# Performance work log

Measured on AMD Instinct MI355X. Metric: run time of the kernel, lower is better.

Reference implementation:

```python
import jax, jax.numpy as jnp
import numpy as np

N, E, R, D = 50000, 640000, 200, 128  # nodes, edges, relations, feat dim (in_feat==out_feat)
EPS = 1e-5  # LayerNorm eps
NEG_SLOPE = 0.01  # F.leaky_relu default

def _xavier(k, shape):
    gain = np.sqrt(2.0)  # calculate_gain('relu')
    std = gain * np.sqrt(2.0 / (shape[0] + shape[1]))
    a = np.sqrt(3.0) * std
    return jax.random.uniform(k, shape, jnp.float32, -a, a)

def setup_inputs() -> dict:
    key = jax.random.key(0)
    ks = jax.random.split(key, 10)
    return {
        "node": jax.random.normal(ks[0], (N, D), jnp.float32),
        "rel": jax.random.normal(ks[1], (R, D), jnp.float32),
        "norm": jax.random.uniform(ks[2], (N, 1), jnp.float32),
        "w_triplet": _xavier(ks[3], (3 * D, D)),
        "w_quad": _xavier(ks[4], (D, D)),
        "loop_weight": _xavier(ks[5], (D, D)),
        "evolve_loop_weight": _xavier(ks[6], (D, D)),
        "src": jax.random.randint(ks[7], (E,), 0, N),
        "dst": jax.random.randint(ks[8], (E,), 0, N),
        "etype": jax.random.randint(ks[9], (E,), 0, R),
    }

def reference(node, rel, norm, w_triplet, w_quad, loop_weight, evolve_loop_weight, src, dst, etype):
    # triplet = cat([h_src, rel_emb, h_dst], 1) @ w_triplet, computed blockwise
    # to avoid materializing the [E, 3D] concat.
    W_s, W_r, W_d = w_triplet[:D], w_triplet[D:2 * D], w_triplet[2 * D:]
    triplet = node[src] @ W_s + rel[etype] @ W_r + node[dst] @ W_d  # [E, D]
    # 'fre' not in edata -> sro_fre is zeros; a_triplet = triplet @ w_quad
    a = jax.nn.leaky_relu(triplet @ w_quad, negative_slope=NEG_SLOPE)  # [E, D]
    # edge_softmax: softmax over incoming edges per destination node, per feature
    a_max = jax.ops.segment_max(a, dst, num_segments=N)
    a_max = jnp.where(jnp.isfinite(a_max), a_max, 0.0)  # empty segments -> -inf
    ex = jnp.exp(a - a_max[dst])
    denom = jax.ops.segment_sum(ex, dst, num_segments=N)
    att = ex / denom[dst]
    # weighted scatter-sum aggregation, then apply_func: h * norm
    h = jax.ops.segment_sum(att * triplet, dst, num_segments=N) * norm  # [N, D]
    # self-loop: evolve_loop_weight for in-degree-0 nodes, loop_weight otherwise
    indeg = jax.ops.segment_sum(jnp.ones((E,), jnp.float32), dst, num_segments=N)
    loop = jnp.where((indeg > 0)[:, None], node @ loop_weight, node @ evolve_loop_weight)
    out = h + loop
    # LayerNorm(elementwise_affine=False)
    mu = jnp.mean(out, axis=-1, keepdims=True)
    var = jnp.var(out, axis=-1, keepdims=True)
    return (out - mu) * jax.lax.rsqrt(var + EPS)
```

## Files before the change

kernel.cpp:

```cpp
#include <hip/hip_runtime.h>
#include <hip/hip_bf16.h>

#define D 128
#define LOG2E 1.4426950408889634f

typedef __attribute__((ext_vector_type(8))) short bf16x8;
typedef __attribute__((ext_vector_type(4))) float f32x4;
typedef __attribute__((ext_vector_type(2))) float f32x2;
typedef __attribute__((ext_vector_type(2))) unsigned u32x2;
typedef __attribute__((ext_vector_type(4))) unsigned u32x4;

__device__ __forceinline__ unsigned short f2bf_bits(float f) {
    union { __hip_bfloat16 h; unsigned short u; } c;
    c.h = __float2bfloat16(f);
    return c.u;
}
__device__ __forceinline__ float bfbits2f(unsigned short u) {
    return __uint_as_float(((unsigned)u) << 16);
}
__device__ __forceinline__ float ldf(const void* p, size_t i, int f32) {
    return f32 ? ((const float*)p)[i] : bfbits2f(((const unsigned short*)p)[i]);
}
__device__ __forceinline__ f32x2 unpk2(unsigned u) {
    f32x2 r;
    r.x = __uint_as_float(u << 16);
    r.y = __uint_as_float(u & 0xFFFF0000u);
    return r;
}
__device__ __forceinline__ f32x2 shx32(f32x2 v) {
    f32x2 r;
    r.x = __shfl_xor(v.x, 32);
    r.y = __shfl_xor(v.y, 32);
    return r;
}
__device__ __forceinline__ f32x2 pk_add(f32x2 a, f32x2 b) {
    f32x2 d;
    asm("v_pk_add_f32 %0, %1, %2" : "=v"(d) : "v"(a), "v"(b));
    return d;
}
__device__ __forceinline__ f32x2 pk_mul(f32x2 a, f32x2 b) {
    f32x2 d;
    asm("v_pk_mul_f32 %0, %1, %2" : "=v"(d) : "v"(a), "v"(b));
    return d;
}
__device__ __forceinline__ f32x2 pk_fma(f32x2 a, f32x2 b, f32x2 c) {
    f32x2 d;
    asm("v_pk_fma_f32 %0, %1, %2, %3" : "=v"(d) : "v"(a), "v"(b), "v"(c));
    return d;
}
__device__ __forceinline__ float fexp2(float x) {
    float r;
    asm("v_exp_f32 %0, %1" : "=v"(r) : "v"(x));
    return r;
}

__global__ __launch_bounds__(256) void prep_kernel(
    const void* __restrict__ node, const void* __restrict__ wtrip,
    const void* __restrict__ wquad, const void* __restrict__ loopW,
    const void* __restrict__ evoW, unsigned short* __restrict__ wT,
    int* __restrict__ cnt, int* __restrict__ rank,
    const int* __restrict__ dst, int* __restrict__ flag, int E) {
    __shared__ int sflag;
    int tid = threadIdx.x;
    int bad = 0;
    if (tid < 64) {
        for (int j = 0; j < 4; j++) {
            float v = bfbits2f(((const unsigned short*)node)[tid + 64 * j]);
            if (!(fabsf(v) < 1e4f)) bad = 1;
        }
    }
    unsigned long long m = __ballot(bad);
    if (tid == 0) sflag = (m != 0ull) ? 1 : 0;
    __syncthreads();
    int f32 = sflag;
    int bx = blockIdx.x;
    if (bx == 0 && tid == 0) *flag = f32;

    if (bx < 192) {
        int unit = bx * 2 + (tid >> 7);
        int k = unit & 127, mjob = unit >> 7;
        int t = tid & 127;
        float acc = 0.f;
        for (int j = 0; j < D; j++)
            acc += ldf(wtrip, (size_t)mjob * D * D + (size_t)k * D + j, f32) *
                   ldf(wquad, (size_t)j * D + t, f32);
        const int jmap0 = (mjob == 0) ? 0 : (mjob == 1 ? 6 : 2);
        wT[(size_t)jmap0 * D * D + (size_t)t * D + k] = f2bf_bits(acc);
    } else if (bx < 272) {
        int u = bx - 192;
        int jr = u >> 4, seg = u & 15;
        const void* srcp; size_t base; int j;
        switch (jr) {
            case 0: srcp = wtrip; base = 0;             j = 1; break;
            case 1: srcp = wtrip; base = 2 * D * D;     j = 3; break;
            case 2: srcp = loopW; base = 0;             j = 4; break;
            case 3: srcp = evoW;  base = 0;             j = 5; break;
            default: srcp = wtrip; base = (size_t)D * D; j = 7; break;
        }
        for (int c = tid; c < 1024; c += 256) {
            int idx = seg * 1024 + c;
            int n = idx >> 7, k = idx & 127;
            unsigned short b = f32 ? f2bf_bits(((const float*)srcp)[base + (size_t)k * D + n])
                                   : ((const unsigned short*)srcp)[base + (size_t)k * D + n];
            wT[(size_t)j * D * D + (size_t)n * D + k] = b;
        }
    } else {
        int e = (bx - 272) * 256 + tid;
        if (e < E) rank[e] = atomicAdd(&cnt[dst[e]], 1);
    }
}

__global__ void scan_block(const int* __restrict__ cnt, int* __restrict__ offs,
                           int* __restrict__ part, int N) {
    __shared__ int sh[256];
    int tid = threadIdx.x;
    int i = blockIdx.x * 256 + tid;
    int v = (i < N) ? cnt[i] : 0;
    sh[tid] = v;
    __syncthreads();
    for (int o = 1; o < 256; o <<= 1) {
        int t = (tid >= o) ? sh[tid - o] : 0;
        __syncthreads();
        sh[tid] += t;
        __syncthreads();
    }
    if (i < N) offs[i] = sh[tid] - v;
    if (tid == 255) part[blockIdx.x] = sh[255];
}

__global__ void scan_fix(int* __restrict__ offs, const int* __restrict__ part,
                         int N, int E) {
    __shared__ int sh[256];
    int tid = threadIdx.x, b = blockIdx.x;
    sh[tid] = (tid < b) ? part[tid] : 0;
    __syncthreads();
    for (int o = 128; o; o >>= 1) {
        if (tid < o) sh[tid] += sh[tid + o];
        __syncthreads();
    }
    int carry = sh[0];
    int i = b * 256 + tid;
    if (i < N) offs[i] += carry;
    if (b == 0 && tid == 0) offs[N] = E;
}

__global__ __launch_bounds__(512) void gemm_kernel(
    const void* __restrict__ node, const void* __restrict__ rel,
    const unsigned short* __restrict__ wT, const int* __restrict__ cnt,
    unsigned* __restrict__ nodeST, unsigned* __restrict__ nodeDT,
    unsigned* __restrict__ relRT, unsigned* __restrict__ loopSel,
    const int* __restrict__ flag, int N, int R, int nodeBlocks,
    const int* __restrict__ src, const int* __restrict__ dst,
    const int* __restrict__ et, const int* __restrict__ offs,
    const int* __restrict__ rank, unsigned* __restrict__ ePack, int E) {
    __shared__ __align__(16) unsigned short Wt[D][D + 8];

    int bx = blockIdx.x, by = blockIdx.y;
    int tid = threadIdx.y * 64 + threadIdx.x;
    int isRel = 0, jp;
    if (bx >= nodeBlocks) {
        if (by == 1) {
            int e = (bx - nodeBlocks) * 512 + tid;
            if (e < E) {
                int d = dst[e];
                ePack[offs[d] + rank[e]] = (unsigned)src[e] | ((unsigned)et[e] << 20);
            }
            return;
        }
        if (by != 0 || bx - nodeBlocks >= (R + 127) / 128) return;
        isRel = 1;
        jp = 3;
    } else {
        jp = by;
    }

    int f32 = *flag;
    int rows = isRel ? R : N;
    int row0 = (isRel ? bx - nodeBlocks : bx) * 128;
    const void* A = isRel ? rel : node;

    int lane = threadIdx.x, wv = threadIdx.y;
    int l16 = lane & 15, quad = lane >> 4;
    int ar = row0 + wv * 16 + l16;
    int ar_c = ar < rows ? ar : rows - 1;

    int qIdx, tIdx;
    unsigned* O = nullptr;
    switch (jp) {
        case 0: qIdx = 0; tIdx = 1; O = nodeST; break;
        case 1: qIdx = 2; tIdx = 3; O = nodeDT; break;
        case 2: qIdx = 4; tIdx = 5; break;
        default: qIdx = 6; tIdx = 7; O = relRT; break;
    }

    bf16x8 af[4];
#pragma unroll
    for (int kk = 0; kk < 4; kk++) {
        int k = kk * 32 + quad * 8;
        if (f32) {
            const float* Af = (const float*)A + (size_t)ar_c * D + k;
            float4 x0 = *(const float4*)(Af);
            float4 x1 = *(const float4*)(Af + 4);
            af[kk][0] = (short)f2bf_bits(x0.x);
            af[kk][1] = (short)f2bf_bits(x0.y);
            af[kk][2] = (short)f2bf_bits(x0.z);
            af[kk][3] = (short)f2bf_bits(x0.w);
            af[kk][4] = (short)f2bf_bits(x1.x);
            af[kk][5] = (short)f2bf_bits(x1.y);
            af[kk][6] = (short)f2bf_bits(x1.z);
            af[kk][7] = (short)f2bf_bits(x1.w);
        } else {
            af[kk] = *(const bf16x8*)((const unsigned short*)A + (size_t)ar_c * D + k);
        }
    }

    const unsigned short* gQ = wT + (size_t)qIdx * D * D;
    const unsigned short* gT = wT + (size_t)tIdx * D * D;

    bf16x8 wreg[4], wreg2[4];
#pragma unroll
    for (int i = 0; i < 4; i++) {
        int c = tid + i * 512;
        wreg[i] = *(const bf16x8*)(gQ + (c >> 4) * 128 + (c & 15) * 8);
    }

    f32x4 accQ[8], accT[8];
#pragma unroll
    for (int i = 0; i < 8; i++) {
        accQ[i] = (f32x4){0.f, 0.f, 0.f, 0.f};
        accT[i] = (f32x4){0.f, 0.f, 0.f, 0.f};
    }

    for (int pass = 0; pass < 2; pass++) {
#pragma unroll
        for (int i = 0; i < 4; i++) {
            int c = tid + i * 512;
            *(bf16x8*)(&Wt[c >> 4][(c & 15) * 8]) = wreg[i];
        }
        if (pass == 0) {
#pragma unroll
            for (int i = 0; i < 4; i++) {
                int c = tid + i * 512;
                wreg2[i] = *(const bf16x8*)(gT + (c >> 4) * 128 + (c & 15) * 8);
            }
        }
        __syncthreads();
        f32x4* acc = pass ? accT : accQ;
#pragma unroll
        for (int kk = 0; kk < 4; kk++) {
#pragma unroll
            for (int nt = 0; nt < 8; nt++) {
                bf16x8 bfr = *(const bf16x8*)(&Wt[nt * 16 + l16][kk * 32 + quad * 8]);
                acc[nt] = __builtin_amdgcn_mfma_f32_16x16x32_bf16(af[kk], bfr, acc[nt], 0, 0, 0);
            }
        }
        __syncthreads();
#pragma unroll
        for (int i = 0; i < 4; i++) wreg[i] = wreg2[i];
    }

    int cr0 = row0 + wv * 16 + quad * 4;
    int odd = l16 & 1;
    if (jp != 2) {
#pragma unroll
        for (int r = 0; r < 4; r++) {
            int cr = cr0 + r;
#pragma unroll
            for (int nt = 0; nt < 8; nt++) {
                float vQ = accQ[nt][r] * LOG2E;
                float vT = accT[nt][r];
                float oQ = __shfl_xor(vQ, 1);
                float oT = __shfl_xor(vT, 1);
                unsigned w;
                if (!odd) w = (unsigned)f2bf_bits(vQ) | ((unsigned)f2bf_bits(oQ) << 16);
                else      w = (unsigned)f2bf_bits(oT) | ((unsigned)f2bf_bits(vT) << 16);
                if (cr < rows) O[(size_t)cr * 128 + nt * 16 + l16] = w;
            }
        }
    } else {
#pragma unroll
        for (int r = 0; r < 4; r++) {
            int cr = cr0 + r;
            int deg = (cr < rows) ? cnt[cr] : 0;
#pragma unroll
            for (int nt = 0; nt < 8; nt++) {
                float vL = accQ[nt][r], vE = accT[nt][r];
                float oL = __shfl_xor(vL, 1);
                float oE = __shfl_xor(vE, 1);
                unsigned wl, we;
                if (!odd) {
                    wl = (unsigned)f2bf_bits(vL) | ((unsigned)f2bf_bits(oL) << 16);
                    we = (unsigned)f2bf_bits(vE) | ((unsigned)f2bf_bits(oE) << 16);
                } else {
                    wl = (unsigned)f2bf_bits(oL) | ((unsigned)f2bf_bits(vL) << 16);
                    we = (unsigned)f2bf_bits(oE) | ((unsigned)f2bf_bits(vE) << 16);
                }
                if (cr < rows && !odd)
                    loopSel[(size_t)cr * 64 + nt * 8 + (l16 >> 1)] = (deg > 0) ? wl : we;
            }
        }
    }
}

__global__ __launch_bounds__(256) void agg_kernel(
    const int* __restrict__ offs, const unsigned* __restrict__ ePack,
    const unsigned* __restrict__ ST, const unsigned* __restrict__ RT,
    const unsigned* __restrict__ DT, const unsigned* __restrict__ loopSel,
    const void* __restrict__ normv, void* __restrict__ out,
    const int* __restrict__ flag, int N) {
    int n = blockIdx.x * 4 + threadIdx.y;
    if (n >= N) return;
    int f32 = *flag;
    int lane = threadIdx.x;
    int half = lane >> 5, sl = lane & 31;
    int start = offs[n], end = offs[n + 1];
    int deg = end - start;

    u32x4 ud = *(const u32x4*)(DT + (size_t)n * 128 + sl * 4);
    f32x2 qd01 = unpk2(ud.x), td01 = unpk2(ud.y);
    f32x2 qd23 = unpk2(ud.z), td23 = unpk2(ud.w);
    u32x2 ul = *(const u32x2*)(loopSel + (size_t)n * 64 + sl * 2);
    f32x2 acc01 = unpk2(ul.x), acc23 = unpk2(ul.y);

    const char* STb = (const char*)ST;
    const char* RTb = (const char*)RT;
    unsigned laneoff = (unsigned)(sl * 16);

    f32x2 den01 = {0.f, 0.f}, den23 = {0.f, 0.f};
    f32x2 h01 = {0.f, 0.f}, h23 = {0.f, 0.f};
    const f32x2 ns2 = {0.01f, 0.01f};

#define GLOAD(PK, US, UR)                                                   \
    u32x4 US = *(const u32x4*)(STb + ((((PK) & 0xFFFFFu) << 9) + laneoff)); \
    u32x4 UR = *(const u32x4*)(RTb + ((((PK) >> 20) << 9) + laneoff));

#define EMATH(US, UR)                                                       \
    {                                                                       \
        f32x2 q01 = pk_add(pk_add(unpk2(US.x), unpk2(UR.x)), qd01);         \
        f32x2 q23 = pk_add(pk_add(unpk2(US.z), unpk2(UR.z)), qd23);         \
        f32x2 s01 = pk_mul(q01, ns2);                                       \
        f32x2 s23 = pk_mul(q23, ns2);                                       \
        f32x2 ex01, ex23;                                                   \
        ex01.x = fexp2(fmaxf(q01.x, s01.x));                                \
        ex01.y = fexp2(fmaxf(q01.y, s01.y));                                \
        ex23.x = fexp2(fmaxf(q23.x, s23.x));                                \
        ex23.y = fexp2(fmaxf(q23.y, s23.y));                                \
        den01 = pk_add(den01, ex01); den23 = pk_add(den23, ex23);           \
        f32x2 t01 = pk_add(pk_add(unpk2(US.y), unpk2(UR.y)), td01);         \
        f32x2 t23 = pk_add(pk_add(unpk2(US.w), unpk2(UR.w)), td23);         \
        h01 = pk_fma(ex01, t01, h01);                                       \
        h23 = pk_fma(ex23, t23, h23);                                       \
    }

#define EMATHV(US, UR, VM)                                                  \
    {                                                                       \
        f32x2 q01 = pk_add(pk_add(unpk2(US.x), unpk2(UR.x)), qd01);         \
        f32x2 q23 = pk_add(pk_add(unpk2(US.z), unpk2(UR.z)), qd23);         \
        f32x2 s01 = pk_mul(q01, ns2);                                       \
        f32x2 s23 = pk_mul(q23, ns2);                                       \
        f32x2 ex01, ex23;                                                   \
        ex01.x = fexp2(fmaxf(q01.x, s01.x)) * (VM);                         \
        ex01.y = fexp2(fmaxf(q01.y, s01.y)) * (VM);                         \
        ex23.x = fexp2(fmaxf(q23.x, s23.x)) * (VM);                         \
        ex23.y = fexp2(fmaxf(q23.y, s23.y)) * (VM);                         \
        den01 = pk_add(den01, ex01); den23 = pk_add(den23, ex23);           \
        f32x2 t01 = pk_add(pk_add(unpk2(US.y), unpk2(UR.y)), td01);         \
        f32x2 t23 = pk_add(pk_add(unpk2(US.w), unpk2(UR.w)), td23);         \
        h01 = pk_fma(ex01, t01, h01);                                       \
        h23 = pk_fma(ex23, t23, h23);                                       \
    }

    int e = start;
    for (; e + 3 < end; e += 4) {
        unsigned pA = ePack[e + half];
        unsigned pB = ePack[e + 2 + half];
        GLOAD(pA, usA, urA)
        GLOAD(pB, usB, urB)
        EMATH(usA, urA)
        EMATH(usB, urB)
    }
    for (; e < end; e += 2) {
        int eh = e + half;
        int valid = eh < end;
        unsigned pT = ePack[valid ? eh : end - 1];
        GLOAD(pT, usT, urT)
        EMATHV(usT, urT, valid ? 1.0f : 0.0f)
    }
#undef GLOAD
#undef EMATH
#undef EMATHV

    den01 = pk_add(den01, shx32(den01)); den23 = pk_add(den23, shx32(den23));
    h01 = pk_add(h01, shx32(h01));       h23 = pk_add(h23, shx32(h23));

    f32x2 x01, x23;
    if (deg > 0) {
        float nrm = ldf(normv, n, f32);
        x01 = h01 / den01 * nrm + acc01;
        x23 = h23 / den23 * nrm + acc23;
    } else {
        x01 = acc01;
        x23 = acc23;
    }

    float s = (x01.x + x01.y) + (x23.x + x23.y);
    float ss = (x01.x * x01.x + x01.y * x01.y) + (x23.x * x23.x + x23.y * x23.y);
#pragma unroll
    for (int o = 16; o; o >>= 1) {
        s += __shfl_xor(s, o);
        ss += __shfl_xor(ss, o);
    }
    float mu = s * (1.f / 128.f);
    float var = ss * (1.f / 128.f) - mu * mu;
    float rstd = rsqrtf(var + 1e-5f);
    f32x2 y01 = (x01 - mu) * rstd;
    f32x2 y23 = (x23 - mu) * rstd;

    if (half == 0) {
        if (f32) {
            float4 o4 = make_float4(y01.x, y01.y, y23.x, y23.y);
            ((float4*)out)[(size_t)n * 32 + sl] = o4;
        } else {
            u32x2 ow;
            ow.x = (unsigned)f2bf_bits(y01.x) | ((unsigned)f2bf_bits(y01.y) << 16);
            ow.y = (unsigned)f2bf_bits(y23.x) | ((unsigned)f2bf_bits(y23.y) << 16);
            *(u32x2*)((unsigned*)out + (size_t)n * 64 + sl * 2) = ow;
        }
    }
}

extern "C" void kernel_launch(void* const* d_in, const int* in_sizes, int n_in,
                              void* d_out, int out_size, void* d_ws, size_t ws_size,
                              hipStream_t stream) {
    const void* node = d_in[0];
    const void* rel = d_in[1];
    const void* normv = d_in[2];
    const void* wtrip = d_in[3];
    const void* wquad = d_in[4];
    const void* loopW = d_in[5];
    const void* evoW = d_in[6];
    const int* src = (const int*)d_in[7];
    const int* dst = (const int*)d_in[8];
    const int* et = (const int*)d_in[9];

    int N = in_sizes[0] / D;
    int R = in_sizes[1] / D;
    int E = in_sizes[7];
    int nb = (N + 255) / 256;
    int nodeBlocks = (N + 127) / 128;
    int relBlocks = (R + 127) / 128;
    int scatBlocks = (E + 511) / 512;

    char* p = (char*)d_ws;
    auto alloc = [&](size_t bytes) -> void* {
        void* r = (void*)p;
        p += (bytes + 255) & ~(size_t)255;
        return r;
    };
    unsigned* nodeST = (unsigned*)alloc((size_t)N * 128 * 4);
    unsigned* nodeDT = (unsigned*)alloc((size_t)N * 128 * 4);
    unsigned* relRT = (unsigned*)alloc((size_t)R * 128 * 4);
    unsigned* loopSel = (unsigned*)alloc((size_t)N * 64 * 4);
    unsigned short* wT = (unsigned short*)alloc((size_t)8 * D * D * 2);
    int* cnt = (int*)alloc((size_t)N * 4);
    int* offs = (int*)alloc((size_t)(N + 1) * 4);
    int* part = (int*)alloc((size_t)(nb + 1) * 4);
    int* rank = (int*)alloc((size_t)E * 4);
    unsigned* ePack = (unsigned*)alloc((size_t)E * 4);
    int* flag = (int*)alloc(4);

    hipMemsetAsync(cnt, 0, (size_t)N * 4, stream);
    prep_kernel<<<272 + (E + 255) / 256, 256, 0, stream>>>(
        node, wtrip, wquad, loopW, evoW, wT, cnt, rank, dst, flag, E);
    scan_block<<<nb, 256, 0, stream>>>(cnt, offs, part, N);
    scan_fix<<<nb, 256, 0, stream>>>(offs, part, N, E);
    int xext = nodeBlocks + (scatBlocks > relBlocks ? scatBlocks : relBlocks);
    gemm_kernel<<<dim3(xext, 3), dim3(64, 8), 0, stream>>>(
        node, rel, wT, cnt, nodeST, nodeDT, relRT, loopSel, flag, N, R, nodeBlocks,
        src, dst, et, offs, rank, ePack, E);
    agg_kernel<<<(N + 3) / 4, dim3(64, 4), 0, stream>>>(
        offs, ePack, nodeST, relRT, nodeDT, loopSel, normv, d_out, flag, N);
}
```

Baseline: 233.6 us.

## Compute all three node projections per block and pre-shift packed edge indices

The gemm kernel now uses a 1D grid. Each node block loads its A-row fragment once and loops over six weight matrices in sequence, writing the ST, DT and loop outputs one after another, instead of launching three separate y-blocks that each reload and convert the node rows. The edge pack grows from 32 to 64 bits and stores the src and etype offsets already shifted, so agg_kernel skips the mask and shift arithmetic per edge. The cost is three times fewer node blocks, each doing three times the work, which lowers parallelism, and twice the bytes for ePack reads and writes.

```diff
diff --git a/kernel.cpp b/kernel.cpp
--- a/kernel.cpp
+++ b/kernel.cpp
@@ -149,30 +149,26 @@
     const unsigned short* __restrict__ wT, const int* __restrict__ cnt,
     unsigned* __restrict__ nodeST, unsigned* __restrict__ nodeDT,
     unsigned* __restrict__ relRT, unsigned* __restrict__ loopSel,
-    const int* __restrict__ flag, int N, int R, int nodeBlocks,
+    const int* __restrict__ flag, int N, int R, int nodeBlocks, int relBlocks,
     const int* __restrict__ src, const int* __restrict__ dst,
     const int* __restrict__ et, const int* __restrict__ offs,
-    const int* __restrict__ rank, unsigned* __restrict__ ePack, int E) {
+    const int* __restrict__ rank, u32x2* __restrict__ ePack, int E) {
     __shared__ __align__(16) unsigned short Wt[D][D + 8];
 
-    int bx = blockIdx.x, by = blockIdx.y;
+    int bx = blockIdx.x;
     int tid = threadIdx.y * 64 + threadIdx.x;
-    int isRel = 0, jp;
-    if (bx >= nodeBlocks) {
-        if (by == 1) {
-            int e = (bx - nodeBlocks) * 512 + tid;
-            if (e < E) {
-                int d = dst[e];
-                ePack[offs[d] + rank[e]] = (unsigned)src[e] | ((unsigned)et[e] << 20);
-            }
-            return;
-        }
-        if (by != 0 || bx - nodeBlocks >= (R + 127) / 128) return;
-        isRel = 1;
-        jp = 3;
-    } else {
-        jp = by;
-    }
+    if (bx >= nodeBlocks + relBlocks) {
+        int e = (bx - nodeBlocks - relBlocks) * 512 + tid;
+        if (e < E) {
+            int d = dst[e];
+            u32x2 pk;
+            pk.x = ((unsigned)src[e]) << 9;
+            pk.y = ((unsigned)et[e]) << 9;
+            ePack[offs[d] + rank[e]] = pk;
+        }
+        return;
+    }
+    int isRel = bx >= nodeBlocks;
 
     int f32 = *flag;
     int rows = isRel ? R : N;
@@ -183,15 +179,6 @@
     int l16 = lane & 15, quad = lane >> 4;
     int ar = row0 + wv * 16 + l16;
     int ar_c = ar < rows ? ar : rows - 1;
-
-    int qIdx, tIdx;
-    unsigned* O = nullptr;
-    switch (jp) {
-        case 0: qIdx = 0; tIdx = 1; O = nodeST; break;
-        case 1: qIdx = 2; tIdx = 3; O = nodeDT; break;
-        case 2: qIdx = 4; tIdx = 5; break;
-        default: qIdx = 6; tIdx = 7; O = relRT; break;
-    }
 
     bf16x8 af[4];
 #pragma unroll
@@ -214,14 +201,14 @@
         }
     }
 
-    const unsigned short* gQ = wT + (size_t)qIdx * D * D;
-    const unsigned short* gT = wT + (size_t)tIdx * D * D;
+    const int base = isRel ? 6 : 0;
+    const int npass = isRel ? 2 : 6;
 
     bf16x8 wreg[4], wreg2[4];
 #pragma unroll
     for (int i = 0; i < 4; i++) {
         int c = tid + i * 512;
-        wreg[i] = *(const bf16x8*)(gQ + (c >> 4) * 128 + (c & 15) * 8);
+        wreg[i] = *(const bf16x8*)(wT + (size_t)base * D * D + (c >> 4) * 128 + (c & 15) * 8);
     }
 
     f32x4 accQ[8], accT[8];
@@ -231,21 +218,25 @@
         accT[i] = (f32x4){0.f, 0.f, 0.f, 0.f};
     }
 
-    for (int pass = 0; pass < 2; pass++) {
+    int cr0 = row0 + wv * 16 + quad * 4;
+    int odd = l16 & 1;
+
+    for (int s = 0; s < npass; s++) {
 #pragma unroll
         for (int i = 0; i < 4; i++) {
             int c = tid + i * 512;
             *(bf16x8*)(&Wt[c >> 4][(c & 15) * 8]) = wreg[i];
         }
-        if (pass == 0) {
+        if (s + 1 < npass) {
+            const unsigned short* gN = wT + (size_t)(base + s + 1) * D * D;
 #pragma unroll
             for (int i = 0; i < 4; i++) {
                 int c = tid + i * 512;
-                wreg2[i] = *(const bf16x8*)(gT + (c >> 4) * 128 + (c & 15) * 8);
+                wreg2[i] = *(const bf16x8*)(gN + (c >> 4) * 128 + (c & 15) * 8);
             }
         }
         __syncthreads();
-        f32x4* acc = pass ? accT : accQ;
+        f32x4* acc = (s & 1) ? accT : accQ;
 #pragma unroll
         for (int kk = 0; kk < 4; kk++) {
 #pragma unroll
@@ -257,53 +248,62 @@
         __syncthreads();
 #pragma unroll
         for (int i = 0; i < 4; i++) wreg[i] = wreg2[i];
-    }
-
-    int cr0 = row0 + wv * 16 + quad * 4;
-    int odd = l16 & 1;
-    if (jp != 2) {
-#pragma unroll
-        for (int r = 0; r < 4; r++) {
-            int cr = cr0 + r;
-#pragma unroll
-            for (int nt = 0; nt < 8; nt++) {
-                float vQ = accQ[nt][r] * LOG2E;
-                float vT = accT[nt][r];
-                float oQ = __shfl_xor(vQ, 1);
-                float oT = __shfl_xor(vT, 1);
-                unsigned w;
-                if (!odd) w = (unsigned)f2bf_bits(vQ) | ((unsigned)f2bf_bits(oQ) << 16);
-                else      w = (unsigned)f2bf_bits(oT) | ((unsigned)f2bf_bits(vT) << 16);
-                if (cr < rows) O[(size_t)cr * 128 + nt * 16 + l16] = w;
+
+        if (s & 1) {
+            int job = s >> 1;
+            if (isRel || job < 2) {
+                unsigned* O = isRel ? relRT : (job == 0 ? nodeST : nodeDT);
+#pragma unroll
+                for (int r = 0; r < 4; r++) {
+                    int cr = cr0 + r;
+#pragma unroll
+                    for (int nt = 0; nt < 8; nt++) {
+                        float vQ = accQ[nt][r] * LOG2E;
+                        float vT = accT[nt][r];
+                        float oQ = __shfl_xor(vQ, 1);
+                        float oT = __shfl_xor(vT, 1);
+                        unsigned w;
+                        if (!odd) w = (unsigned)f2bf_bits(vQ) | ((unsigned)f2bf_bits(oQ) << 16);
+                        else      w = (unsigned)f2bf_bits(oT) | ((unsigned)f2bf_bits(vT) << 16);
+                        if (cr < rows) O[(size_t)cr * 128 + nt * 16 + l16] = w;
+                    }
+                }
+            } else {
+#pragma unroll
+                for (int r = 0; r < 4; r++) {
+                    int cr = cr0 + r;
+                    int deg = (cr < rows) ? cnt[cr] : 0;
+#pragma unroll
+                    for (int nt = 0; nt < 8; nt++) {
+                        float vL = accQ[nt][r], vE = accT[nt][r];
+                        float oL = __shfl_xor(vL, 1);
+                        float oE = __shfl_xor(vE, 1);
+                        unsigned wl, we;
+                        if (!odd) {
+                            wl = (unsigned)f2bf_bits(vL) | ((unsigned)f2bf_bits(oL) << 16);
+                            we = (unsigned)f2bf_bits(vE) | ((unsigned)f2bf_bits(oE) << 16);
+                        } else {
+                            wl = (unsigned)f2bf_bits(oL) | ((unsigned)f2bf_bits(vL) << 16);
+                            we = (unsigned)f2bf_bits(oE) | ((unsigned)f2bf_bits(vE) << 16);
+                        }
+                        if (cr < rows && !odd)
+                            loopSel[(size_t)cr * 64 + nt * 8 + (l16 >> 1)] = (deg > 0) ? wl : we;
+                    }
+                }
             }
-        }
-    } else {
-#pragma unroll
-        for (int r = 0; r < 4; r++) {
-            int cr = cr0 + r;
-            int deg = (cr < rows) ? cnt[cr] : 0;
-#pragma unroll
-            for (int nt = 0; nt < 8; nt++) {
-                float vL = accQ[nt][r], vE = accT[nt][r];
-                float oL = __shfl_xor(vL, 1);
-                float oE = __shfl_xor(vE, 1);
-                unsigned wl, we;
-                if (!odd) {
-                    wl = (unsigned)f2bf_bits(vL) | ((unsigned)f2bf_bits(oL) << 16);
-                    we = (unsigned)f2bf_bits(vE) | ((unsigned)f2bf_bits(oE) << 16);
-                } else {
-                    wl = (unsigned)f2bf_bits(oL) | ((unsigned)f2bf_bits(vL) << 16);
-                    we = (unsigned)f2bf_bits(oE) | ((unsigned)f2bf_bits(vE) << 16);
+            if (s + 1 < npass) {
+#pragma unroll
+                for (int i = 0; i < 8; i++) {
+                    accQ[i] = (f32x4){0.f, 0.f, 0.f, 0.f};
+                    accT[i] = (f32x4){0.f, 0.f, 0.f, 0.f};
                 }
-                if (cr < rows && !odd)
-                    loopSel[(size_t)cr * 64 + nt * 8 + (l16 >> 1)] = (deg > 0) ? wl : we;
             }
         }
     }
 }
 
 __global__ __launch_bounds__(256) void agg_kernel(
-    const int* __restrict__ offs, const unsigned* __restrict__ ePack,
+    const int* __restrict__ offs, const u32x2* __restrict__ ePack,
     const unsigned* __restrict__ ST, const unsigned* __restrict__ RT,
     const unsigned* __restrict__ DT, const unsigned* __restrict__ loopSel,
     const void* __restrict__ normv, void* __restrict__ out,
@@ -331,8 +331,8 @@
     const f32x2 ns2 = {0.01f, 0.01f};
 
 #define GLOAD(PK, US, UR)                                                   \
-    u32x4 US = *(const u32x4*)(STb + ((((PK) & 0xFFFFFu) << 9) + laneoff)); \
-    u32x4 UR = *(const u32x4*)(RTb + ((((PK) >> 20) << 9) + laneoff));
+    u32x4 US = *(const u32x4*)(STb + (size_t)((PK).x + laneoff));           \
+    u32x4 UR = *(const u32x4*)(RTb + (size_t)((PK).y + laneoff));
 
 #define EMATH(US, UR)                                                       \
     {                                                                       \
@@ -372,8 +372,8 @@
 
     int e = start;
     for (; e + 3 < end; e += 4) {
-        unsigned pA = ePack[e + half];
-        unsigned pB = ePack[e + 2 + half];
+        u32x2 pA = ePack[e + half];
+        u32x2 pB = ePack[e + 2 + half];
         GLOAD(pA, usA, urA)
         GLOAD(pB, usB, urB)
         EMATH(usA, urA)
@@ -382,7 +382,7 @@
     for (; e < end; e += 2) {
         int eh = e + half;
         int valid = eh < end;
-        unsigned pT = ePack[valid ? eh : end - 1];
+        u32x2 pT = ePack[valid ? eh : end - 1];
         GLOAD(pT, usT, urT)
         EMATHV(usT, urT, valid ? 1.0f : 0.0f)
     }
@@ -466,7 +466,7 @@
     int* offs = (int*)alloc((size_t)(N + 1) * 4);
     int* part = (int*)alloc((size_t)(nb + 1) * 4);
     int* rank = (int*)alloc((size_t)E * 4);
-    unsigned* ePack = (unsigned*)alloc((size_t)E * 4);
+    u32x2* ePack = (u32x2*)alloc((size_t)E * 8);
     int* flag = (int*)alloc(4);
 
     hipMemsetAsync(cnt, 0, (size_t)N * 4, stream);
@@ -474,10 +474,9 @@
         node, wtrip, wquad, loopW, evoW, wT, cnt, rank, dst, flag, E);
     scan_block<<<nb, 256, 0, stream>>>(cnt, offs, part, N);
     scan_fix<<<nb, 256, 0, stream>>>(offs, part, N, E);
-    int xext = nodeBlocks + (scatBlocks > relBlocks ? scatBlocks : relBlocks);
-    gemm_kernel<<<dim3(xext, 3), dim3(64, 8), 0, stream>>>(
+    gemm_kernel<<<nodeBlocks + relBlocks + scatBlocks, dim3(64, 8), 0, stream>>>(
         node, rel, wT, cnt, nodeST, nodeDT, relRT, loopSel, flag, N, R, nodeBlocks,
-        src, dst, et, offs, rank, ePack, E);
+        relBlocks, src, dst, et, offs, rank, ePack, E);
     agg_kernel<<<(N + 3) / 4, dim3(64, 4), 0, stream>>>(
         offs, ePack, nodeST, relRT, nodeDT, loopSel, normv, d_out, flag, N);
 }
```

Measured after the change: 241.3 us. 3.3% more time.
